# Performance work log

Measured on AMD Instinct MI355X. Metric: run time of the kernel, lower is better.

The kernel has to match this reference:

```python
import math
import jax, jax.numpy as jnp
import numpy as np

N_HEADS = 16


def setup_inputs() -> dict:
    key = jax.random.key(0)
    k1, k2 = jax.random.split(key)
    N, H, C, T = 2, N_HEADS, 64, 2048
    qkv = jax.random.normal(k1, (N, H * 3 * C, T), dtype=jnp.float32)
    mask = jax.random.randint(k2, (N, 1, T), 0, 2).astype(bool) | (jnp.arange(T)[None, None, :] < T // 2)
    return {"qkv": qkv, "mask": mask}


def reference(qkv, mask):
    bs, width, length = qkv.shape
    ch = width // (3 * N_HEADS)
    qkv_r = qkv.reshape(bs * N_HEADS, 3 * ch, length)
    q, k, v = qkv_r[:, :ch], qkv_r[:, ch:2 * ch], qkv_r[:, 2 * ch:]
    scale = 1.0 / math.sqrt(math.sqrt(ch))
    # [bH, T, T] scores in float32 (matches weight.float())
    weight = jnp.einsum('bct,bcs->bts', q * scale, k * scale).astype(jnp.float32)
    inv = ~mask[:, 0, :]                                   # [N, T] True = pad
    m = inv[:, None, :] | inv[:, :, None]                  # [N, T, T]
    m = jnp.broadcast_to(m[:, None], (bs, N_HEADS, length, length)).reshape(-1, length, length)
    weight = jnp.where(m, jnp.finfo(weight.dtype).min, weight)
    weight = jax.nn.softmax(weight, axis=-1)
    a = jnp.einsum('bts,bcs->bct', weight, v)              # [bH, C, T]
    return a.reshape(bs, -1, length)
```

## Files before the change

### kernel.cpp

```cpp
#include <hip/hip_runtime.h>
#include <hip/hip_bf16.h>
#include <stdint.h>

namespace {

constexpr int T_LEN = 2048;
constexpr int NROWS = 192;
constexpr int QBLK  = 64;
constexpr int NBH   = 32;
constexpr int KT_STRIDE = 72;
constexpr int TILE_ELEMS = 64 * KT_STRIDE;
constexpr int TILE_BYTES = TILE_ELEMS * 2;

typedef float f32x4 __attribute__((ext_vector_type(4)));
typedef short bf16x8 __attribute__((ext_vector_type(8)));
typedef short bf16x4 __attribute__((ext_vector_type(4)));

__device__ __forceinline__ unsigned short f2bf(float f) {
  union { float f; unsigned u; } v; v.f = f;
  unsigned r = v.u + 0x7fffu + ((v.u >> 16) & 1u);
  return (unsigned short)(r >> 16);
}
__device__ __forceinline__ unsigned pack2(float a, float b) {
  return (unsigned)f2bf(a) | ((unsigned)f2bf(b) << 16);
}
__device__ __forceinline__ float fast_exp2(float x) {
#if __has_builtin(__builtin_amdgcn_exp2f)
  return __builtin_amdgcn_exp2f(x);
#else
  return exp2f(x);
#endif
}
__device__ __forceinline__ f32x4 mfma_16x16x16_bf16(bf16x4 a, bf16x4 b, f32x4 c) {
#if __has_builtin(__builtin_amdgcn_mfma_f32_16x16x16bf16_1k)
  return __builtin_amdgcn_mfma_f32_16x16x16bf16_1k(a, b, c, 0, 0, 0);
#else
  asm("v_mfma_f32_16x16x16_bf16 %0, %1, %2, %0" : "+v"(c) : "v"(a), "v"(b));
  return c;
#endif
}
__device__ __forceinline__ void gload_lds16(const void* g, void* l) {
  __builtin_amdgcn_global_load_lds(
      (const __attribute__((address_space(1))) unsigned int*)g,
      (__attribute__((address_space(3))) unsigned int*)l, 16, 0, 0);
}

}

__global__ void nm_kernel(const unsigned char* __restrict__ raw,
                          unsigned char* __restrict__ outm, int n) {
  int stride = (raw[1] != 0) ? 1 : ((raw[4] != 0) ? 4 : 8);
  int i = blockIdx.x * blockDim.x + threadIdx.x;
  if (i < n) outm[i] = (raw[(size_t)i * stride] != 0) ? 1 : 0;
}

__global__ void bias9_kernel(const unsigned char* __restrict__ raw,
                             float* __restrict__ bias, int n) {
  int stride = (raw[1] != 0) ? 1 : ((raw[4] != 0) ? 4 : 8);
  int i = blockIdx.x * blockDim.x + threadIdx.x;
  if (i < n) bias[i] = (raw[(size_t)i * stride] != 0) ? 0.0f : -1.0e30f;
  else if (i < n + T_LEN) bias[i] = 0.0f;
}


__global__ __launch_bounds__(256) void tq9_kernel(const float* __restrict__ qkv,
                                                  const unsigned char* __restrict__ mraw,
                                                  short* __restrict__ qtg,
                                                  short* __restrict__ ktg) {
  __shared__ float tile[64][65];
  const int t = threadIdx.x;
  const int which = blockIdx.z;
  const int bh = blockIdx.y;
  const int bx = blockIdx.x;
  const int s0 = bx * 64;
  const float* src = qkv + (size_t)bh * NROWS * T_LEN + (size_t)which * 64 * T_LEN;
  const int c = t >> 2;
  #pragma unroll
  for (int p = 0; p < 4; ++p) {
    int col = (t & 3) * 4 + p * 16;
    float4 v = *(const float4*)&src[(size_t)c * T_LEN + s0 + col];
    tile[c][col] = v.x; tile[c][col + 1] = v.y;
    tile[c][col + 2] = v.z; tile[c][col + 3] = v.w;
  }
  __syncthreads();
  const int s = t & 63;
  float scale;
  if (which) {
    scale = 1.0f;
  } else {
    const int mstride = (mraw[1] != 0) ? 1 : ((mraw[4] != 0) ? 4 : 8);
    const int nb = bh >> 4;
    const bool live = mraw[((size_t)nb * T_LEN + s0 + s) * mstride] != 0;
    scale = live ? 0.18033688011112042f : 0.0f;
  }
  #pragma unroll
  for (int p = 0; p < 2; ++p) {
    int jc = (t >> 6) * 2 + p;
    bf16x4 o0, o1;
    #pragma unroll
    for (int i = 0; i < 4; ++i) {
      o0[i] = (short)f2bf(tile[jc * 8 + i][s] * scale);
      o1[i] = (short)f2bf(tile[jc * 8 + 4 + i][s] * scale);
    }
    short* d = which
      ? (ktg + (size_t)(bh * 32 + bx) * TILE_ELEMS + s * KT_STRIDE + jc * 8)
      : (qtg + (size_t)bh * T_LEN * 64 + (size_t)(s0 + s) * 64 + jc * 8);
    *(bf16x4*)d = o0;
    *(bf16x4*)(d + 4) = o1;
  }
}

__global__ __launch_bounds__(256) void cv3_kernel(const float* __restrict__ qkv,
                                                  short* __restrict__ vtg) {
  int cid = blockIdx.x * 256 + threadIdx.x;
  int bh = cid >> 14;
  int rem = cid & 16383;
  int c = rem >> 8;
  int cg = rem & 255;
  int grp = cg >> 3, jin = cg & 7;
  const float* src = qkv + (size_t)bh * NROWS * T_LEN + (size_t)(128 + c) * T_LEN + cg * 8;
  float4 a = *(const float4*)src;
  float4 b = *(const float4*)(src + 4);
  bf16x4 o0, o1;
  o0[0] = (short)f2bf(a.x); o0[1] = (short)f2bf(a.y);
  o0[2] = (short)f2bf(a.z); o0[3] = (short)f2bf(a.w);
  o1[0] = (short)f2bf(b.x); o1[1] = (short)f2bf(b.y);
  o1[2] = (short)f2bf(b.z); o1[3] = (short)f2bf(b.w);
  short* d = vtg + (size_t)(bh * 32 + grp) * TILE_ELEMS + c * KT_STRIDE + jin * 8;
  *(bf16x4*)d = o0;
  *(bf16x4*)(d + 4) = o1;
}


__global__ __launch_bounds__(512) void attn9_kernel(const short* __restrict__ qtg,
                                                    const short* __restrict__ ktg,
                                                    const short* __restrict__ vtg,
                                                    const float* __restrict__ bias,
                                                    int mask_elems,
                                                    float* __restrict__ out) {
  __shared__ __align__(16) short Kt[2][TILE_ELEMS];
  __shared__ __align__(16) short Vs[2][TILE_ELEMS];

  const int tid  = threadIdx.x;
  const int lane = tid & 63;
  const int wv   = tid >> 6;
  const int tw   = wv & 3;
  const int sh   = wv >> 2;
  const int l15  = lane & 15;
  const int g    = lane >> 4;

  int id = blockIdx.x;
  id = (id & 7) * 128 + (id >> 3);
  const int bh = id >> 5;
  const int t0 = (id & 31) * QBLK;
  const int nb = bh >> 4;

  const int t_lane = t0 + tw * 16 + l15;
  const short* Qrow = qtg + (size_t)bh * T_LEN * 64 + (size_t)t_lane * 64;
  const bf16x8 qf0 = *(const bf16x8*)(Qrow + g * 8);
  const bf16x8 qf1 = *(const bf16x8*)(Qrow + 32 + g * 8);

  const float bt = bias[(size_t)nb * T_LEN + t_lane];
  const float* __restrict__ brow = bias + ((bt != 0.0f) ? (size_t)mask_elems
                                                        : (size_t)nb * T_LEN);

  const char* __restrict__ kt0 = (const char*)(ktg + (size_t)bh * 32 * TILE_ELEMS);
  const char* __restrict__ vt0 = (const char*)(vtg + (size_t)bh * 32 * TILE_ELEMS);

  gload_lds16(kt0 + wv * 1024 + lane * 16, (char*)Kt[0] + wv * 1024);
  gload_lds16(vt0 + wv * 1024 + lane * 16, (char*)Vs[0] + wv * 1024);
  if (wv == 0) gload_lds16(kt0 + 8192 + lane * 16, (char*)Kt[0] + 8192);
  if (wv == 1) gload_lds16(vt0 + 8192 + lane * 16, (char*)Vs[0] + 8192);
  __syncthreads();

  f32x4 acc[4];
  #pragma unroll
  for (int i = 0; i < 4; ++i) acc[i] = (f32x4){0.f, 0.f, 0.f, 0.f};
  float l_part = 0.0f;

  int cur = 0;
  for (int sb = 0; sb < T_LEN / 64; ++sb) {
    if (sb + 1 < T_LEN / 64) {
      const char* ks = kt0 + (size_t)(sb + 1) * TILE_BYTES;
      const char* vs = vt0 + (size_t)(sb + 1) * TILE_BYTES;
      char* Ktn = (char*)Kt[cur ^ 1];
      char* Vsn = (char*)Vs[cur ^ 1];
      gload_lds16(ks + wv * 1024 + lane * 16, Ktn + wv * 1024);
      gload_lds16(vs + wv * 1024 + lane * 16, Vsn + wv * 1024);
      if (wv == 0) gload_lds16(ks + 8192 + lane * 16, Ktn + 8192);
      if (wv == 1) gload_lds16(vs + 8192 + lane * 16, Vsn + 8192);
    }

    const short* Ktc = Kt[cur];
    const short* Vsc = Vs[cur];
    const int s0 = sb * 64;
    #pragma unroll
    for (int sti = 0; sti < 2; ++sti) {
      const int st = sh * 2 + sti;
      const int srow = st * 16 + l15;
      bf16x8 kf0 = *(const bf16x8*)&Ktc[srow * KT_STRIDE + g * 8];
      bf16x8 kf1 = *(const bf16x8*)&Ktc[srow * KT_STRIDE + 32 + g * 8];
      f32x4 S = (f32x4){0.f, 0.f, 0.f, 0.f};
      S = __builtin_amdgcn_mfma_f32_16x16x32_bf16(kf0, qf0, S, 0, 0, 0);
      S = __builtin_amdgcn_mfma_f32_16x16x32_bf16(kf1, qf1, S, 0, 0, 0);

      const f32x4 b4 = *(const f32x4*)&brow[s0 + st * 16 + g * 4];
      float p0 = fast_exp2(S[0] + b4[0]);
      float p1 = fast_exp2(S[1] + b4[1]);
      float p2 = fast_exp2(S[2] + b4[2]);
      float p3 = fast_exp2(S[3] + b4[3]);
      l_part += (p0 + p1) + (p2 + p3);

      union { bf16x4 v; __hip_bfloat162 h[2]; } pf;
      pf.h[0] = __float22bfloat162_rn(float2{p0, p1});
      pf.h[1] = __float22bfloat162_rn(float2{p2, p3});

      #pragma unroll
      for (int cb = 0; cb < 4; ++cb) {
        bf16x4 vf = *(const bf16x4*)&Vsc[(cb * 16 + l15) * KT_STRIDE + st * 16 + g * 4];
        acc[cb] = mfma_16x16x16_bf16(vf, pf.v, acc[cb]);
      }
    }

    __syncthreads();
    cur ^= 1;
  }

  float* scratch = (float*)Kt;
  const int trow = tw * 16 + l15;
  if (wv >= 4) {
    float* row = scratch + trow * 68;
    #pragma unroll
    for (int cb = 0; cb < 4; ++cb) *(f32x4*)&row[cb * 16 + g * 4] = acc[cb];
    row[64 + g] = l_part;
  }
  __syncthreads();
  if (wv < 4) {
    const float* row = scratch + trow * 68;
    #pragma unroll
    for (int cb = 0; cb < 4; ++cb) acc[cb] += *(const f32x4*)&row[cb * 16 + g * 4];
    l_part += row[64 + g];

    l_part += __shfl_xor(l_part, 16, 64);
    l_part += __shfl_xor(l_part, 32, 64);
    const float il = 1.0f / l_part;
    const size_t out_base = (size_t)bh * 64 * T_LEN;
    #pragma unroll
    for (int cb = 0; cb < 4; ++cb) {
      #pragma unroll
      for (int r = 0; r < 4; ++r) {
        int c = cb * 16 + g * 4 + r;
        out[out_base + (size_t)c * T_LEN + t_lane] = acc[cb][r] * il;
      }
    }
  }
}


__global__ __launch_bounds__(256) void attn_fb_kernel(const float* __restrict__ qkv,
                                                      const unsigned char* __restrict__ maskn,
                                                      float* __restrict__ out) {
  __shared__ __align__(16) short Kt[QBLK * KT_STRIDE];
  __shared__ __align__(16) short Vs[64 * KT_STRIDE];
  __shared__ __align__(16) unsigned char Ms[T_LEN];

  const int tid  = threadIdx.x;
  const int lane = tid & 63;
  const int wv   = tid >> 6;
  const int l15  = lane & 15;
  const int g    = lane >> 4;

  const int bh = blockIdx.y;
  const int nb = bh >> 4;
  const int t0 = blockIdx.x * QBLK;

  const float* __restrict__ Qg = qkv + (size_t)bh * NROWS * T_LEN;
  const float* __restrict__ Kg = Qg + (size_t)64 * T_LEN;
  const float* __restrict__ Vg = Qg + (size_t)128 * T_LEN;

  {
    const uint2* src = (const uint2*)(maskn + (size_t)nb * T_LEN);
    ((uint2*)Ms)[tid] = src[tid];
  }
  {
    const int c2 = (tid >> 6) * 2;
    const int s  = tid & 63;
    #pragma unroll
    for (int p = 0; p < 8; ++p) {
      int c = p * 8 + c2;
      float f0 = Qg[(size_t)c * T_LEN + t0 + s] * 0.125f;
      float f1 = Qg[(size_t)(c + 1) * T_LEN + t0 + s] * 0.125f;
      *(unsigned*)&Kt[s * KT_STRIDE + c] = pack2(f0, f1);
    }
  }
  __syncthreads();

  bf16x8 qf0 = *(const bf16x8*)&Kt[(wv * 16 + l15) * KT_STRIDE + g * 8];
  bf16x8 qf1 = *(const bf16x8*)&Kt[(wv * 16 + l15) * KT_STRIDE + 32 + g * 8];
  const int t_lane = t0 + wv * 16 + l15;
  const bool invt = (Ms[t_lane] == 0);

  f32x4 acc[4];
  #pragma unroll
  for (int i = 0; i < 4; ++i) acc[i] = (f32x4){0.f, 0.f, 0.f, 0.f};
  float m_run = -3.0e38f;
  float l_run = 0.0f;

  for (int sb = 0; sb < T_LEN / 64; ++sb) {
    const int s0 = sb * 64;
    __syncthreads();
    {
      const int c2 = (tid >> 6) * 2;
      const int s  = tid & 63;
      #pragma unroll
      for (int p = 0; p < 8; ++p) {
        int c = p * 8 + c2;
        float f0 = Kg[(size_t)c * T_LEN + s0 + s];
        float f1 = Kg[(size_t)(c + 1) * T_LEN + s0 + s];
        *(unsigned*)&Kt[s * KT_STRIDE + c] = pack2(f0, f1);
      }
    }
    {
      const int cv = (tid >> 5);
      const int s2 = tid & 31;
      #pragma unroll
      for (int p = 0; p < 8; ++p) {
        int c = p * 8 + cv;
        float2 f = *(const float2*)&Vg[(size_t)c * T_LEN + s0 + 2 * s2];
        *(unsigned*)&Vs[c * KT_STRIDE + 2 * s2] = pack2(f.x, f.y);
      }
    }
    __syncthreads();

    #pragma unroll
    for (int st = 0; st < 4; ++st) {
      const int srow = st * 16 + l15;
      bf16x8 kf0 = *(const bf16x8*)&Kt[srow * KT_STRIDE + g * 8];
      bf16x8 kf1 = *(const bf16x8*)&Kt[srow * KT_STRIDE + 32 + g * 8];
      f32x4 S = (f32x4){0.f, 0.f, 0.f, 0.f};
      S = __builtin_amdgcn_mfma_f32_16x16x32_bf16(kf0, qf0, S, 0, 0, 0);
      S = __builtin_amdgcn_mfma_f32_16x16x32_bf16(kf1, qf1, S, 0, 0, 0);

      const unsigned m4 = *(const unsigned*)&Ms[s0 + st * 16 + g * 4];
      float vals[4];
      #pragma unroll
      for (int r = 0; r < 4; ++r) {
        float x = ((m4 >> (8 * r)) & 0xffu) ? S[r] : -1.0e30f;
        vals[r] = invt ? 0.0f : x;
      }
      float pm = fmaxf(fmaxf(vals[0], vals[1]), fmaxf(vals[2], vals[3]));
      pm = fmaxf(pm, __shfl_xor(pm, 16, 64));
      pm = fmaxf(pm, __shfl_xor(pm, 32, 64));
      const float newm = fmaxf(m_run, pm);
      const float alpha = fast_exp2((m_run - newm) * 1.44269504f);
      float p0 = fast_exp2((vals[0] - newm) * 1.44269504f);
      float p1 = fast_exp2((vals[1] - newm) * 1.44269504f);
      float p2 = fast_exp2((vals[2] - newm) * 1.44269504f);
      float p3 = fast_exp2((vals[3] - newm) * 1.44269504f);
      float ps = (p0 + p1) + (p2 + p3);
      ps += __shfl_xor(ps, 16, 64);
      ps += __shfl_xor(ps, 32, 64);
      l_run = l_run * alpha + ps;
      m_run = newm;
      if (__any(alpha < 1.0f)) {
        #pragma unroll
        for (int cb = 0; cb < 4; ++cb)
          #pragma unroll
          for (int r = 0; r < 4; ++r) acc[cb][r] *= alpha;
      }
      bf16x4 pf;
      pf[0] = (short)f2bf(p0); pf[1] = (short)f2bf(p1);
      pf[2] = (short)f2bf(p2); pf[3] = (short)f2bf(p3);
      #pragma unroll
      for (int cb = 0; cb < 4; ++cb) {
        bf16x4 vf = *(const bf16x4*)&Vs[(cb * 16 + l15) * KT_STRIDE + st * 16 + g * 4];
        acc[cb] = mfma_16x16x16_bf16(vf, pf, acc[cb]);
      }
    }
  }

  const float il = 1.0f / l_run;
  const size_t out_base = (size_t)bh * 64 * T_LEN;
  #pragma unroll
  for (int cb = 0; cb < 4; ++cb) {
    #pragma unroll
    for (int r = 0; r < 4; ++r) {
      int c = cb * 16 + g * 4 + r;
      out[out_base + (size_t)c * T_LEN + t_lane] = acc[cb][r] * il;
    }
  }
}


extern "C" void kernel_launch(void* const* d_in, const int* in_sizes, int n_in,
                              void* d_out, int out_size, void* d_ws, size_t ws_size,
                              hipStream_t stream) {
  (void)n_in; (void)out_size;
  const float* qkv = (const float*)d_in[0];
  const unsigned char* mraw = (const unsigned char*)d_in[1];
  float* out = (float*)d_out;
  const int mask_elems = in_sizes[1];

  const size_t QSZ = (size_t)NBH * T_LEN * 64 * sizeof(short);
  const size_t TSZ = (size_t)NBH * 32 * TILE_ELEMS * sizeof(short);
  const size_t BSZ = (size_t)(mask_elems + T_LEN) * sizeof(float);
  const size_t need = QSZ + 2 * TSZ + BSZ;
  if (ws_size >= need) {
    short* qtg = (short*)d_ws;
    short* ktg = (short*)((char*)d_ws + QSZ);
    short* vtg = (short*)((char*)d_ws + QSZ + TSZ);
    float* bias = (float*)((char*)d_ws + QSZ + 2 * TSZ);
    bias9_kernel<<<(mask_elems + T_LEN + 255) / 256, 256, 0, stream>>>(mraw, bias, mask_elems);
    tq9_kernel<<<dim3(T_LEN / 64, NBH, 2), 256, 0, stream>>>(qkv, mraw, qtg, ktg);
    cv3_kernel<<<(NBH * 64 * 256) / 256, 256, 0, stream>>>(qkv, vtg);
    attn9_kernel<<<dim3(NBH * 32), 512, 0, stream>>>(qtg, ktg, vtg, bias, mask_elems, out);
  } else {
    unsigned char* maskn = (unsigned char*)d_ws;
    nm_kernel<<<(mask_elems + 255) / 256, 256, 0, stream>>>(mraw, maskn, mask_elems);
    attn_fb_kernel<<<dim3(T_LEN / QBLK, NBH), 256, 0, stream>>>(qkv, maskn, out);
  }
}
```

Before: 91.37 us.

## Repartition attention waves so each K/V fragment serves two query tiles

New measurement: 92.14 us. Within noise of the previous version (+0.8%).

```diff
diff --git a/kernel.cpp b/kernel.cpp
--- a/kernel.cpp
+++ b/kernel.cpp
@@ -132,20 +132,19 @@
 }
 
 
-__global__ __launch_bounds__(512) void attn9_kernel(const short* __restrict__ qtg,
-                                                    const short* __restrict__ ktg,
-                                                    const short* __restrict__ vtg,
-                                                    const float* __restrict__ bias,
-                                                    int mask_elems,
-                                                    float* __restrict__ out) {
-  __shared__ __align__(16) short Kt[2][TILE_ELEMS];
-  __shared__ __align__(16) short Vs[2][TILE_ELEMS];
+__global__ __launch_bounds__(512, 4) void attn11_kernel(const short* __restrict__ qtg,
+                                                        const short* __restrict__ ktg,
+                                                        const short* __restrict__ vtg,
+                                                        const float* __restrict__ bias,
+                                                        int mask_elems,
+                                                        float* __restrict__ out) {
+  __shared__ __align__(16) short smem[4 * TILE_ELEMS];
 
   const int tid  = threadIdx.x;
   const int lane = tid & 63;
   const int wv   = tid >> 6;
-  const int tw   = wv & 3;
-  const int sh   = wv >> 2;
+  const int sgrp = wv & 3;
+  const int tgrp = wv >> 2;
   const int l15  = lane & 15;
   const int g    = lane >> 4;
 
@@ -155,102 +154,154 @@
   const int t0 = (id & 31) * QBLK;
   const int nb = bh >> 4;
 
-  const int t_lane = t0 + tw * 16 + l15;
-  const short* Qrow = qtg + (size_t)bh * T_LEN * 64 + (size_t)t_lane * 64;
-  const bf16x8 qf0 = *(const bf16x8*)(Qrow + g * 8);
-  const bf16x8 qf1 = *(const bf16x8*)(Qrow + 32 + g * 8);
-
-  const float bt = bias[(size_t)nb * T_LEN + t_lane];
-  const float* __restrict__ brow = bias + ((bt != 0.0f) ? (size_t)mask_elems
-                                                        : (size_t)nb * T_LEN);
+  const int tA = t0 + (tgrp * 2) * 16 + l15;
+  const int tB = tA + 16;
+
+  const short* Qbase = qtg + (size_t)bh * T_LEN * 64;
+  const bf16x8 qfA0 = *(const bf16x8*)(Qbase + (size_t)tA * 64 + g * 8);
+  const bf16x8 qfA1 = *(const bf16x8*)(Qbase + (size_t)tA * 64 + 32 + g * 8);
+  const bf16x8 qfB0 = *(const bf16x8*)(Qbase + (size_t)tB * 64 + g * 8);
+  const bf16x8 qfB1 = *(const bf16x8*)(Qbase + (size_t)tB * 64 + 32 + g * 8);
+
+  const float btA = bias[(size_t)nb * T_LEN + tA];
+  const float btB = bias[(size_t)nb * T_LEN + tB];
+  const float* __restrict__ browA = bias + ((btA != 0.0f) ? (size_t)mask_elems
+                                                          : (size_t)nb * T_LEN);
+  const float* __restrict__ browB = bias + ((btB != 0.0f) ? (size_t)mask_elems
+                                                          : (size_t)nb * T_LEN);
 
   const char* __restrict__ kt0 = (const char*)(ktg + (size_t)bh * 32 * TILE_ELEMS);
   const char* __restrict__ vt0 = (const char*)(vtg + (size_t)bh * 32 * TILE_ELEMS);
-
-  gload_lds16(kt0 + wv * 1024 + lane * 16, (char*)Kt[0] + wv * 1024);
-  gload_lds16(vt0 + wv * 1024 + lane * 16, (char*)Vs[0] + wv * 1024);
-  if (wv == 0) gload_lds16(kt0 + 8192 + lane * 16, (char*)Kt[0] + 8192);
-  if (wv == 1) gload_lds16(vt0 + 8192 + lane * 16, (char*)Vs[0] + 8192);
+  char* KtL = (char*)smem;
+  char* VsL = (char*)(smem + 2 * TILE_ELEMS);
+
+  gload_lds16(kt0 + wv * 1024 + lane * 16, KtL + wv * 1024);
+  gload_lds16(vt0 + wv * 1024 + lane * 16, VsL + wv * 1024);
+  if (wv == 0) gload_lds16(kt0 + 8192 + lane * 16, KtL + 8192);
+  if (wv == 1) gload_lds16(vt0 + 8192 + lane * 16, VsL + 8192);
   __syncthreads();
 
-  f32x4 acc[4];
+  f32x4 accA[4], accB[4];
   #pragma unroll
-  for (int i = 0; i < 4; ++i) acc[i] = (f32x4){0.f, 0.f, 0.f, 0.f};
-  float l_part = 0.0f;
+  for (int i = 0; i < 4; ++i) { accA[i] = (f32x4){0.f,0.f,0.f,0.f}; accB[i] = accA[i]; }
+  float lA = 0.0f, lB = 0.0f;
+
+  const int koff = (sgrp * 16 + l15) * KT_STRIDE;
+  const int boff = sgrp * 16 + g * 4;
 
   int cur = 0;
   for (int sb = 0; sb < T_LEN / 64; ++sb) {
     if (sb + 1 < T_LEN / 64) {
       const char* ks = kt0 + (size_t)(sb + 1) * TILE_BYTES;
       const char* vs = vt0 + (size_t)(sb + 1) * TILE_BYTES;
-      char* Ktn = (char*)Kt[cur ^ 1];
-      char* Vsn = (char*)Vs[cur ^ 1];
+      char* Ktn = KtL + (cur ^ 1) * TILE_BYTES;
+      char* Vsn = VsL + (cur ^ 1) * TILE_BYTES;
       gload_lds16(ks + wv * 1024 + lane * 16, Ktn + wv * 1024);
       gload_lds16(vs + wv * 1024 + lane * 16, Vsn + wv * 1024);
       if (wv == 0) gload_lds16(ks + 8192 + lane * 16, Ktn + 8192);
       if (wv == 1) gload_lds16(vs + 8192 + lane * 16, Vsn + 8192);
     }
 
-    const short* Ktc = Kt[cur];
-    const short* Vsc = Vs[cur];
-    const int s0 = sb * 64;
-    #pragma unroll
-    for (int sti = 0; sti < 2; ++sti) {
-      const int st = sh * 2 + sti;
-      const int srow = st * 16 + l15;
-      bf16x8 kf0 = *(const bf16x8*)&Ktc[srow * KT_STRIDE + g * 8];
-      bf16x8 kf1 = *(const bf16x8*)&Ktc[srow * KT_STRIDE + 32 + g * 8];
-      f32x4 S = (f32x4){0.f, 0.f, 0.f, 0.f};
-      S = __builtin_amdgcn_mfma_f32_16x16x32_bf16(kf0, qf0, S, 0, 0, 0);
-      S = __builtin_amdgcn_mfma_f32_16x16x32_bf16(kf1, qf1, S, 0, 0, 0);
-
-      const f32x4 b4 = *(const f32x4*)&brow[s0 + st * 16 + g * 4];
-      float p0 = fast_exp2(S[0] + b4[0]);
-      float p1 = fast_exp2(S[1] + b4[1]);
-      float p2 = fast_exp2(S[2] + b4[2]);
-      float p3 = fast_exp2(S[3] + b4[3]);
-      l_part += (p0 + p1) + (p2 + p3);
-
-      union { bf16x4 v; __hip_bfloat162 h[2]; } pf;
-      pf.h[0] = __float22bfloat162_rn(float2{p0, p1});
-      pf.h[1] = __float22bfloat162_rn(float2{p2, p3});
-
-      #pragma unroll
-      for (int cb = 0; cb < 4; ++cb) {
-        bf16x4 vf = *(const bf16x4*)&Vsc[(cb * 16 + l15) * KT_STRIDE + st * 16 + g * 4];
-        acc[cb] = mfma_16x16x16_bf16(vf, pf.v, acc[cb]);
-      }
-    }
-
-    __syncthreads();
-    cur ^= 1;
-  }
-
-  float* scratch = (float*)Kt;
-  const int trow = tw * 16 + l15;
-  if (wv >= 4) {
-    float* row = scratch + trow * 68;
-    #pragma unroll
-    for (int cb = 0; cb < 4; ++cb) *(f32x4*)&row[cb * 16 + g * 4] = acc[cb];
-    row[64 + g] = l_part;
-  }
-  __syncthreads();
-  if (wv < 4) {
-    const float* row = scratch + trow * 68;
-    #pragma unroll
-    for (int cb = 0; cb < 4; ++cb) acc[cb] += *(const f32x4*)&row[cb * 16 + g * 4];
-    l_part += row[64 + g];
-
-    l_part += __shfl_xor(l_part, 16, 64);
-    l_part += __shfl_xor(l_part, 32, 64);
-    const float il = 1.0f / l_part;
-    const size_t out_base = (size_t)bh * 64 * T_LEN;
+    const short* Ktc = smem + cur * TILE_ELEMS;
+    const short* Vsc = smem + (2 + cur) * TILE_ELEMS;
+
+    bf16x8 kf0 = *(const bf16x8*)&Ktc[koff + g * 8];
+    bf16x8 kf1 = *(const bf16x8*)&Ktc[koff + 32 + g * 8];
+
+    f32x4 SA = (f32x4){0.f, 0.f, 0.f, 0.f};
+    SA = __builtin_amdgcn_mfma_f32_16x16x32_bf16(kf0, qfA0, SA, 0, 0, 0);
+    SA = __builtin_amdgcn_mfma_f32_16x16x32_bf16(kf1, qfA1, SA, 0, 0, 0);
+    f32x4 SB = (f32x4){0.f, 0.f, 0.f, 0.f};
+    SB = __builtin_amdgcn_mfma_f32_16x16x32_bf16(kf0, qfB0, SB, 0, 0, 0);
+    SB = __builtin_amdgcn_mfma_f32_16x16x32_bf16(kf1, qfB1, SB, 0, 0, 0);
+
+    const f32x4 b4A = *(const f32x4*)&browA[sb * 64 + boff];
+    const f32x4 b4B = *(const f32x4*)&browB[sb * 64 + boff];
+    float pA0 = fast_exp2(SA[0] + b4A[0]);
+    float pA1 = fast_exp2(SA[1] + b4A[1]);
+    float pA2 = fast_exp2(SA[2] + b4A[2]);
+    float pA3 = fast_exp2(SA[3] + b4A[3]);
+    lA += (pA0 + pA1) + (pA2 + pA3);
+    float pB0 = fast_exp2(SB[0] + b4B[0]);
+    float pB1 = fast_exp2(SB[1] + b4B[1]);
+    float pB2 = fast_exp2(SB[2] + b4B[2]);
+    float pB3 = fast_exp2(SB[3] + b4B[3]);
+    lB += (pB0 + pB1) + (pB2 + pB3);
+
+    union { bf16x4 v; __hip_bfloat162 h[2]; } pfA, pfB;
+    pfA.h[0] = __float22bfloat162_rn(float2{pA0, pA1});
+    pfA.h[1] = __float22bfloat162_rn(float2{pA2, pA3});
+    pfB.h[0] = __float22bfloat162_rn(float2{pB0, pB1});
+    pfB.h[1] = __float22bfloat162_rn(float2{pB2, pB3});
+
     #pragma unroll
     for (int cb = 0; cb < 4; ++cb) {
-      #pragma unroll
-      for (int r = 0; r < 4; ++r) {
-        int c = cb * 16 + g * 4 + r;
-        out[out_base + (size_t)c * T_LEN + t_lane] = acc[cb][r] * il;
+      bf16x4 vf = *(const bf16x4*)&Vsc[(cb * 16 + l15) * KT_STRIDE + sgrp * 16 + g * 4];
+      accA[cb] = mfma_16x16x16_bf16(vf, pfA.v, accA[cb]);
+      accB[cb] = mfma_16x16x16_bf16(vf, pfB.v, accB[cb]);
+    }
+
+    __syncthreads();
+    cur ^= 1;
+  }
+
+  float* scr = (float*)smem;
+  {
+    const int lb = lane * 36;
+    if (sgrp >= 2) {
+      float* base = scr + ((sgrp - 2) * 2 + tgrp) * 2304 + lb;
+      #pragma unroll
+      for (int cb = 0; cb < 4; ++cb) {
+        *(f32x4*)&base[cb * 4] = accA[cb];
+        *(f32x4*)&base[16 + cb * 4] = accB[cb];
+      }
+      base[32] = lA; base[33] = lB;
+    }
+    __syncthreads();
+    if (sgrp < 2) {
+      const float* base = scr + (sgrp * 2 + tgrp) * 2304 + lb;
+      #pragma unroll
+      for (int cb = 0; cb < 4; ++cb) {
+        accA[cb] += *(const f32x4*)&base[cb * 4];
+        accB[cb] += *(const f32x4*)&base[16 + cb * 4];
+      }
+      lA += base[32]; lB += base[33];
+    }
+    __syncthreads();
+    if (sgrp == 1) {
+      float* base = scr + tgrp * 2304 + lb;
+      #pragma unroll
+      for (int cb = 0; cb < 4; ++cb) {
+        *(f32x4*)&base[cb * 4] = accA[cb];
+        *(f32x4*)&base[16 + cb * 4] = accB[cb];
+      }
+      base[32] = lA; base[33] = lB;
+    }
+    __syncthreads();
+    if (sgrp == 0) {
+      const float* base = scr + tgrp * 2304 + lb;
+      #pragma unroll
+      for (int cb = 0; cb < 4; ++cb) {
+        accA[cb] += *(const f32x4*)&base[cb * 4];
+        accB[cb] += *(const f32x4*)&base[16 + cb * 4];
+      }
+      lA += base[32]; lB += base[33];
+
+      lA += __shfl_xor(lA, 16, 64);
+      lA += __shfl_xor(lA, 32, 64);
+      lB += __shfl_xor(lB, 16, 64);
+      lB += __shfl_xor(lB, 32, 64);
+      const float ilA = 1.0f / lA;
+      const float ilB = 1.0f / lB;
+      const size_t out_base = (size_t)bh * 64 * T_LEN;
+      #pragma unroll
+      for (int cb = 0; cb < 4; ++cb) {
+        #pragma unroll
+        for (int r = 0; r < 4; ++r) {
+          int c = cb * 16 + g * 4 + r;
+          out[out_base + (size_t)c * T_LEN + tA] = accA[cb][r] * ilA;
+          out[out_base + (size_t)c * T_LEN + tB] = accB[cb][r] * ilB;
+        }
       }
     }
   }
@@ -413,7 +464,7 @@
     bias9_kernel<<<(mask_elems + T_LEN + 255) / 256, 256, 0, stream>>>(mraw, bias, mask_elems);
     tq9_kernel<<<dim3(T_LEN / 64, NBH, 2), 256, 0, stream>>>(qkv, mraw, qtg, ktg);
     cv3_kernel<<<(NBH * 64 * 256) / 256, 256, 0, stream>>>(qkv, vtg);
-    attn9_kernel<<<dim3(NBH * 32), 512, 0, stream>>>(qtg, ktg, vtg, bias, mask_elems, out);
+    attn11_kernel<<<dim3(NBH * 32), 512, 0, stream>>>(qtg, ktg, vtg, bias, mask_elems, out);
   } else {
     unsigned char* maskn = (unsigned char*)d_ws;
     nm_kernel<<<(mask_elems + 255) / 256, 256, 0, stream>>>(mraw, maskn, mask_elems);
```
